# Kernel tuning notes

Hardware: AMD Instinct MI355X
Metric: run time of the kernel (lower is better)

## Reference

```python
import jax, jax.numpy as jnp
import numpy as np
from jax import lax

B, CIN, COUT, H, W, K = 32, 256, 256, 56, 56, 3

def setup_inputs() -> dict:
    key = jax.random.key(0)
    k1, k2, k3 = jax.random.split(key, 3)
    inp = jax.random.normal(k1, (B, CIN, H, W), dtype=jnp.float32)
    # kaiming-style init for conv kernel, normal init for bias
    fan_in = CIN * K * K
    kernel = jax.random.normal(k2, (COUT, CIN, K, K), dtype=jnp.float32) * np.float32(np.sqrt(2.0 / fan_in))
    bias = jax.random.normal(k3, (COUT,), dtype=jnp.float32)
    return {"inp": inp, "kernel": kernel, "bias": bias}

def reference(inp, kernel, bias):
    # Equivalent to the crossbar path: im2col 3x3 patches @ stacked [kernel|bias]
    # matrix == standard conv2d(padding=1, stride=1) + bias.
    out = lax.conv_general_dilated(
        inp, kernel,
        window_strides=(1, 1),
        padding=((1, 1), (1, 1)),
        dimension_numbers=("NCHW", "OIHW", "NCHW"),
    )
    return out + bias[None, :, None, None]
```

## Files before the change

### kernel.cpp

```cpp
#include <hip/hip_runtime.h>
#include <hip/hip_bf16.h>


#define BB    32
#define CINC  256
#define COUTC 256
#define HH    56
#define WW    56
#define HP    58
#define WP    58
#define PIX_PER_IMG 3136
#define NPIX  100352
#define KTOT  2304
#define NKT   72

#define XT_BYTES ((size_t)BB*HP*WP*CINC*2)
#define AWR_FRAGS (72*16*64)
#define AWR_BYTES ((size_t)AWR_FRAGS*16)

#define BUF_SZ 8192

using frag_t = __attribute__((ext_vector_type(8))) short;
using f32x4  = __attribute__((ext_vector_type(4))) float;

__device__ __forceinline__ void gload_lds16(const void* gsrc, void* ldst) {
  __builtin_amdgcn_global_load_lds(
      (const __attribute__((address_space(1))) unsigned*)gsrc,
      (__attribute__((address_space(3))) unsigned*)ldst, 16, 0, 0);
}

__global__ void xpose_kernel(const float* __restrict__ inp,
                             __hip_bfloat16* __restrict__ xt) {
  int bid = blockIdx.x;
  int hp = bid % HP;
  int t  = bid / HP;
  int cb = t % 4;
  int b  = t / 4;
  __shared__ __hip_bfloat16 tile[64 * 60];
  int tid = threadIdx.x;
  for (int i = tid; i < 64 * 60; i += 256) tile[i] = __float2bfloat16(0.f);
  __syncthreads();
  int h = hp - 1;
  if (h >= 0 && h < HH) {
    const float* src = inp + ((size_t)(b * CINC + cb * 64) * HH + h) * WW;
    for (int i = tid; i < 64 * WW; i += 256) {
      int ci = i / WW, w = i - ci * WW;
      tile[ci * 60 + (w + 1)] = __float2bfloat16(src[(size_t)ci * HH * WW + w]);
    }
  }
  __syncthreads();
  __hip_bfloat16* dst = xt + ((size_t)(b * HP + hp) * WP) * CINC + cb * 64;
  for (int i = tid; i < WP * 64; i += 256) {
    int wp = i >> 6, ci = i & 63;
    dst[(size_t)wp * CINC + ci] = tile[ci * 60 + wp];
  }
}

__global__ void wprep_pack(const float* __restrict__ k4,
                           frag_t* __restrict__ awr) {
  int i = blockIdx.x * 256 + threadIdx.x;
  if (i >= AWR_FRAGS) return;
  int lane = i & 63;
  int mb   = (i >> 6) & 15;
  int t    = i >> 10;
  int co   = mb * 16 + (lane & 15);
  int kb   = t * 32 + (lane >> 4) * 8;
  frag_t v;
#pragma unroll
  for (int j = 0; j < 8; ++j) {
    int k = kb + j;
    int tap = k >> 8;
    int ci  = k & 255;
    __hip_bfloat16 h = __float2bfloat16(k4[(co * CINC + ci) * 9 + tap]);
    v[j] = *reinterpret_cast<short*>(&h);
  }
  awr[i] = v;
}

__global__ __launch_bounds__(256, 3) void conv_occ(
    const __hip_bfloat16* __restrict__ xt,
    const frag_t* __restrict__ awr,
    const float* __restrict__ bias,
    float* __restrict__ out) {
  __shared__ alignas(16) char lds[3 * BUF_SZ];

  const int tid  = threadIdx.x;
  const int lane = tid & 63;
  const int wid  = tid >> 6;
  const int wm   = wid >> 1;
  const int wn   = wid & 1;
  const int fr   = lane & 15;
  const int g    = lane >> 4;

  const int bid   = blockIdx.x;
  const int wgid  = (bid & 7) * 196 + (bid >> 3);
  const int ctile = wgid & 1;
  const int ptile = wgid >> 1;

  const char* xt_b = (const char*)xt;

  const int lr  = lane >> 2;
  const int sc  = ((((lane & 3) - ((lane >> 3) & 3)) & 3) << 4);

  auto mkB = [&](int jb) -> const char* {
    int px = ptile * 128 + wid * 32 + jb * 16 + lr;
    int b  = px / PIX_PER_IMG;
    int hw = px - b * PIX_PER_IMG;
    int h = hw / WW, w = hw - h * WW;
    return xt_b + (size_t)((b * HP + h) * WP + w) * (CINC * 2) + sc;
  };
  const char* pB0 = mkB(0);
  const char* pB1 = mkB(1);

#define STG(T2, WB) {                                                      \
    int _tap = (T2) >> 3; int _rr = _tap / 3, _ss = _tap - _rr * 3;        \
    size_t _bo = (size_t)(_rr * WP + _ss) * (CINC * 2)                     \
               + (size_t)((T2) & 7) * 64;                                  \
    char* _d = lds + (WB) * BUF_SZ;                                        \
    gload_lds16(pB0 + _bo, _d + wid * 2048 + 0);                           \
    gload_lds16(pB1 + _bo, _d + wid * 2048 + 1024); }

  const frag_t* abase = awr + (size_t)(ctile * 8 + wm * 4) * 64 + lane;

#define ALOAD(T1, FA) {                                                    \
    const frag_t* _p = abase + (size_t)(T1) * (16 * 64);                   \
    _Pragma("unroll") for (int m = 0; m < 4; ++m)                          \
      FA[m] = _p[m * 64]; }

  const int ckr   = (((g + (fr >> 1)) & 3) << 4);
  const int broff = (wn * 64 + fr) * 64 + ckr;

  frag_t fa0[4], fa1[4], fb[4];
  f32x4 acc[4][4] = {};

#define RSL(RB) {                                                          \
    const char* _b = lds + (RB) * BUF_SZ;                                  \
    _Pragma("unroll") for (int n = 0; n < 4; ++n)                          \
      fb[n] = *(const frag_t*)(_b + broff + n * 1024); }

#define MF(FA) {                                                           \
    __builtin_amdgcn_s_setprio(1);                                         \
    _Pragma("unroll") for (int m = 0; m < 4; ++m)                          \
    _Pragma("unroll") for (int n = 0; n < 4; ++n)                          \
      acc[m][n] = __builtin_amdgcn_mfma_f32_16x16x32_bf16(                 \
          FA[m], fb[n], acc[m][n], 0, 0, 0);                               \
    __builtin_amdgcn_s_setprio(0); }

#define BODY(T, RB, WB, FCUR, FNXT) {                                      \
    STG((T) + 2, WB);                                                      \
    ALOAD((T) + 1, FNXT);                                                  \
    RSL(RB);                                                               \
    MF(FCUR);                                                              \
    asm volatile("s_waitcnt vmcnt(6)" ::: "memory");                       \
    __builtin_amdgcn_s_barrier();                                          \
    __builtin_amdgcn_sched_barrier(0); }

  STG(0, 0);
  STG(1, 1);
  ALOAD(0, fa0);
  asm volatile("s_waitcnt vmcnt(6)" ::: "memory");
  __builtin_amdgcn_s_barrier();
  __builtin_amdgcn_sched_barrier(0);

  for (int base = 0; base < 66; base += 6) {
    BODY(base + 0, 0, 2, fa0, fa1);
    BODY(base + 1, 1, 0, fa1, fa0);
    BODY(base + 2, 2, 1, fa0, fa1);
    BODY(base + 3, 0, 2, fa1, fa0);
    BODY(base + 4, 1, 0, fa0, fa1);
    BODY(base + 5, 2, 1, fa1, fa0);
  }
  BODY(66, 0, 2, fa0, fa1);
  BODY(67, 1, 0, fa1, fa0);
  BODY(68, 2, 1, fa0, fa1);
  BODY(69, 0, 2, fa1, fa0);

  {
    ALOAD(71, fa1);
    RSL(1);
    MF(fa0);
    asm volatile("s_waitcnt vmcnt(0)" ::: "memory");
    __builtin_amdgcn_s_barrier();
    __builtin_amdgcn_sched_barrier(0);
  }
  {
    RSL(2);
    MF(fa1);
  }

  int pb[4], phw[4];
#pragma unroll
  for (int n = 0; n < 4; ++n) {
    int pxg = ptile * 128 + wn * 64 + n * 16 + fr;
    pb[n]  = pxg / PIX_PER_IMG;
    phw[n] = pxg - pb[n] * PIX_PER_IMG;
  }
#pragma unroll
  for (int m = 0; m < 4; ++m) {
#pragma unroll
    for (int rg = 0; rg < 4; ++rg) {
      int co = ctile * 128 + wm * 64 + m * 16 + g * 4 + rg;
      float bv = bias[co];
#pragma unroll
      for (int n = 0; n < 4; ++n)
        out[((size_t)pb[n] * COUTC + co) * PIX_PER_IMG + phw[n]] =
            acc[m][n][rg] + bv;
    }
  }
}

__global__ void conv_direct(const float* __restrict__ inp,
                            const float* __restrict__ kern,
                            const float* __restrict__ bias,
                            float* __restrict__ out) {
  int idx = blockIdx.x * 256 + threadIdx.x;
  if (idx >= BB * COUTC * PIX_PER_IMG) return;
  int w = idx % WW;
  int t = idx / WW;
  int h = t % HH; t /= HH;
  int co = t % COUTC;
  int b  = t / COUTC;
  float acc = bias[co];
  for (int ci = 0; ci < CINC; ++ci)
    for (int r = 0; r < 3; ++r) {
      int hh = h + r - 1;
      if (hh < 0 || hh >= HH) continue;
      for (int s = 0; s < 3; ++s) {
        int ww2 = w + s - 1;
        if (ww2 < 0 || ww2 >= WW) continue;
        acc += inp[((size_t)(b * CINC + ci) * HH + hh) * WW + ww2] *
               kern[(co * CINC + ci) * 9 + r * 3 + s];
      }
    }
  out[idx] = acc;
}

extern "C" void kernel_launch(void* const* d_in, const int* in_sizes, int n_in,
                              void* d_out, int out_size, void* d_ws, size_t ws_size,
                              hipStream_t stream) {
  const float* inp  = (const float*)d_in[0];
  const float* kern = (const float*)d_in[1];
  const float* bias = (const float*)d_in[2];
  float* out = (float*)d_out;

  size_t need = XT_BYTES + AWR_BYTES;
  if (ws_size < need) {
    int tot = BB * COUTC * PIX_PER_IMG;
    conv_direct<<<(tot + 255) / 256, 256, 0, stream>>>(inp, kern, bias, out);
    return;
  }

  __hip_bfloat16* xt = (__hip_bfloat16*)d_ws;
  frag_t* awr = (frag_t*)((char*)d_ws + XT_BYTES);

  xpose_kernel<<<BB * 4 * HP, 256, 0, stream>>>(inp, xt);
  wprep_pack<<<(AWR_FRAGS + 255) / 256, 256, 0, stream>>>(kern, awr);
  conv_occ<<<2 * (NPIX / 128), 256, 0, stream>>>(xt, awr, bias, out);
}
```

Measured before the change: 184.8 us.

## Give each wave a private B-tile ring to drop workgroup barriers

Each wave now stages its own copy of the 64-pixel B slab it consumes into a private 3-slot LDS ring, instead of sharing a block-wide buffer. Because no wave reads another wave's data, the per-k-step s_barrier is removed and only a per-wave vmcnt wait is kept. The cost is that the waves sharing a wn index load the same B data twice, doubling global-to-LDS traffic for B, and LDS use grows to 48KB per block, which may limit occupancy. The epilogue is folded into the main loop by clamping the prefetch indices, so the last iterations issue redundant loads.

```diff
diff --git a/kernel.cpp b/kernel.cpp
--- a/kernel.cpp
+++ b/kernel.cpp
@@ -18,7 +18,8 @@
 #define AWR_FRAGS (72*16*64)
 #define AWR_BYTES ((size_t)AWR_FRAGS*16)
 
-#define BUF_SZ 8192
+#define RING   4096
+#define WLDS   (3*RING)
 
 using frag_t = __attribute__((ext_vector_type(8))) short;
 using f32x4  = __attribute__((ext_vector_type(4))) float;
@@ -77,12 +78,12 @@
   awr[i] = v;
 }
 
-__global__ __launch_bounds__(256, 3) void conv_occ(
+__global__ __launch_bounds__(256, 3) void conv_free(
     const __hip_bfloat16* __restrict__ xt,
     const frag_t* __restrict__ awr,
     const float* __restrict__ bias,
     float* __restrict__ out) {
-  __shared__ alignas(16) char lds[3 * BUF_SZ];
+  __shared__ alignas(16) char lds[4 * WLDS];
 
   const int tid  = threadIdx.x;
   const int lane = tid & 63;
@@ -98,12 +99,13 @@
   const int ptile = wgid >> 1;
 
   const char* xt_b = (const char*)xt;
+  char* wbase = lds + wid * WLDS;
 
   const int lr  = lane >> 2;
   const int sc  = ((((lane & 3) - ((lane >> 3) & 3)) & 3) << 4);
 
   auto mkB = [&](int jb) -> const char* {
-    int px = ptile * 128 + wid * 32 + jb * 16 + lr;
+    int px = ptile * 128 + wn * 64 + jb * 16 + lr;
     int b  = px / PIX_PER_IMG;
     int hw = px - b * PIX_PER_IMG;
     int h = hw / WW, w = hw - h * WW;
@@ -111,14 +113,18 @@
   };
   const char* pB0 = mkB(0);
   const char* pB1 = mkB(1);
+  const char* pB2 = mkB(2);
+  const char* pB3 = mkB(3);
 
 #define STG(T2, WB) {                                                      \
     int _tap = (T2) >> 3; int _rr = _tap / 3, _ss = _tap - _rr * 3;        \
     size_t _bo = (size_t)(_rr * WP + _ss) * (CINC * 2)                     \
                + (size_t)((T2) & 7) * 64;                                  \
-    char* _d = lds + (WB) * BUF_SZ;                                        \
-    gload_lds16(pB0 + _bo, _d + wid * 2048 + 0);                           \
-    gload_lds16(pB1 + _bo, _d + wid * 2048 + 1024); }
+    char* _d = wbase + (WB) * RING;                                        \
+    gload_lds16(pB0 + _bo, _d + 0);                                        \
+    gload_lds16(pB1 + _bo, _d + 1024);                                     \
+    gload_lds16(pB2 + _bo, _d + 2048);                                     \
+    gload_lds16(pB3 + _bo, _d + 3072); }
 
   const frag_t* abase = awr + (size_t)(ctile * 8 + wm * 4) * 64 + lane;
 
@@ -128,13 +134,13 @@
       FA[m] = _p[m * 64]; }
 
   const int ckr   = (((g + (fr >> 1)) & 3) << 4);
-  const int broff = (wn * 64 + fr) * 64 + ckr;
+  const int broff = fr * 64 + ckr;
 
   frag_t fa0[4], fa1[4], fb[4];
   f32x4 acc[4][4] = {};
 
 #define RSL(RB) {                                                          \
-    const char* _b = lds + (RB) * BUF_SZ;                                  \
+    const char* _b = wbase + (RB) * RING;                                  \
     _Pragma("unroll") for (int n = 0; n < 4; ++n)                          \
       fb[n] = *(const frag_t*)(_b + broff + n * 1024); }
 
@@ -147,45 +153,26 @@
     __builtin_amdgcn_s_setprio(0); }
 
 #define BODY(T, RB, WB, FCUR, FNXT) {                                      \
-    STG((T) + 2, WB);                                                      \
-    ALOAD((T) + 1, FNXT);                                                  \
+    int _t1 = (T) + 1 <= 71 ? (T) + 1 : 71;                                \
+    int _t2 = (T) + 2 <= 71 ? (T) + 2 : 71;                                \
+    ALOAD(_t1, FNXT);                                                      \
+    STG(_t2, WB);                                                          \
+    asm volatile("s_waitcnt vmcnt(12)" ::: "memory");                      \
+    __builtin_amdgcn_sched_barrier(0);                                     \
     RSL(RB);                                                               \
-    MF(FCUR);                                                              \
-    asm volatile("s_waitcnt vmcnt(6)" ::: "memory");                       \
-    __builtin_amdgcn_s_barrier();                                          \
-    __builtin_amdgcn_sched_barrier(0); }
-
+    MF(FCUR); }
+
+  ALOAD(0, fa0);
   STG(0, 0);
   STG(1, 1);
-  ALOAD(0, fa0);
-  asm volatile("s_waitcnt vmcnt(6)" ::: "memory");
-  __builtin_amdgcn_s_barrier();
-  __builtin_amdgcn_sched_barrier(0);
-
-  for (int base = 0; base < 66; base += 6) {
+
+  for (int base = 0; base < 72; base += 6) {
     BODY(base + 0, 0, 2, fa0, fa1);
     BODY(base + 1, 1, 0, fa1, fa0);
     BODY(base + 2, 2, 1, fa0, fa1);
     BODY(base + 3, 0, 2, fa1, fa0);
     BODY(base + 4, 1, 0, fa0, fa1);
     BODY(base + 5, 2, 1, fa1, fa0);
-  }
-  BODY(66, 0, 2, fa0, fa1);
-  BODY(67, 1, 0, fa1, fa0);
-  BODY(68, 2, 1, fa0, fa1);
-  BODY(69, 0, 2, fa1, fa0);
-
-  {
-    ALOAD(71, fa1);
-    RSL(1);
-    MF(fa0);
-    asm volatile("s_waitcnt vmcnt(0)" ::: "memory");
-    __builtin_amdgcn_s_barrier();
-    __builtin_amdgcn_sched_barrier(0);
-  }
-  {
-    RSL(2);
-    MF(fa1);
   }
 
   int pb[4], phw[4];
@@ -255,5 +242,5 @@
 
   xpose_kernel<<<BB * 4 * HP, 256, 0, stream>>>(inp, xt);
   wprep_pack<<<(AWR_FRAGS + 255) / 256, 256, 0, stream>>>(kern, awr);
-  conv_occ<<<2 * (NPIX / 128), 256, 0, stream>>>(xt, awr, bias, out);
-}
+  conv_free<<<2 * (NPIX / 128), 256, 0, stream>>>(xt, awr, bias, out);
+}
```

Result: slower. 219.7 us (+18.9%).
